# Optimization experiments

Hardware: AMD Instinct MI355X
Metric: run time of the kernel (lower is better)

## Reference

```python
import jax, jax.numpy as jnp
import numpy as np

N_EXPERTS = 64
TOP_K = 8
ALPHA = 0.01
EMBED_DIM = 2048


def setup_inputs() -> dict:
    key = jax.random.key(0)
    k1, k2 = jax.random.split(key)
    hidden_states = jax.random.normal(k1, (4, 8192, EMBED_DIM), dtype=jnp.float32)
    # router weight, torch init-style scale
    weight = jax.random.normal(k2, (N_EXPERTS, EMBED_DIM), dtype=jnp.float32) / np.sqrt(EMBED_DIM)
    return {"hidden_states": hidden_states, "weight": weight}


def reference(hidden_states, weight):
    # flatten tokens: [B,S,D] -> [N,D]
    x = hidden_states.reshape(-1, hidden_states.shape[-1])
    # router logits: [N,E]
    logits = jnp.einsum('nd,ed->ne', x, weight)
    scores = jax.nn.softmax(logits, axis=-1)
    # top-k routing weights and expert ids (torch uses sorted=False; order is immaterial)
    topk_weight, topk_idx = jax.lax.top_k(scores, TOP_K)
    # aux load-balance loss (training path, alpha > 0)
    counts = jnp.bincount(topk_idx.reshape(-1), length=N_EXPERTS).astype(scores.dtype)
    ce = counts / topk_idx.size  # fraction of assignments per expert
    Pi = scores.mean(axis=0)     # mean router prob per expert
    aux_loss = jnp.sum(Pi * ce * N_EXPERTS) * ALPHA
    return topk_idx, topk_weight, aux_loss
```

## Files before the change

### kernel.cpp

```cpp
#include <hip/hip_runtime.h>

#define EMBED_D  2048
#define N_EXP    64
#define K_TOP    8
#define TOK_BLK  64
#define THREADS  256
#define NCHUNK   64
#define WCHUNK_B 12288
#define XCHUNK_B 8192
#define BUF_B    (WCHUNK_B + XCHUNK_B)

typedef __attribute__((ext_vector_type(8))) short bf16x8;
typedef __attribute__((ext_vector_type(4))) float f32x4;

__device__ __forceinline__ uint bf16_rne(float x) {
    uint u = __float_as_uint(x);
    return (u + 0x7fffu + ((u >> 16) & 1u)) >> 16;
}
__device__ __forceinline__ float bf16f(uint h) { return __uint_as_float(h << 16); }

__device__ __forceinline__ void stage16(const void* g, void* l)
{
    typedef __attribute__((address_space(1))) const unsigned int gu32;
    typedef __attribute__((address_space(3))) unsigned int lu32;
    __builtin_amdgcn_global_load_lds((gu32*)g, (lu32*)l, 16, 0, 0);
}

__device__ __forceinline__ void split3(float4 u, float4 v, bf16x8& H, bf16x8& M, bf16x8& L)
{
    const float x[8] = {u.x, u.y, u.z, u.w, v.x, v.y, v.z, v.w};
    uint hw[8], mw[8], lw[8];
#pragma unroll
    for (int j = 0; j < 8; ++j) {
        const uint ux = __float_as_uint(x[j]);
        hw[j] = (ux + 0x7fffu + ((ux >> 16) & 1u)) & 0xffff0000u;
        const float r1 = x[j] - __uint_as_float(hw[j]);
        const uint ur = __float_as_uint(r1);
        mw[j] = (ur + 0x7fffu + ((ur >> 16) & 1u)) & 0xffff0000u;
        lw[j] = __float_as_uint(r1 - __uint_as_float(mw[j]));
    }
    uint* hp = (uint*)&H; uint* mp = (uint*)&M; uint* lp = (uint*)&L;
#pragma unroll
    for (int w = 0; w < 4; ++w) {
        hp[w] = __builtin_amdgcn_perm(hw[2 * w + 1], hw[2 * w], 0x07060302u);
        mp[w] = __builtin_amdgcn_perm(mw[2 * w + 1], mw[2 * w], 0x07060302u);
        lp[w] = __builtin_amdgcn_perm(lw[2 * w + 1], lw[2 * w], 0x07060302u);
    }
}

__global__ void w_prep(const float* __restrict__ W, ushort* __restrict__ WF)
{
    const int e = blockIdx.x;
    const int t = threadIdx.x;
    const float4 a = *(const float4*)(W + (size_t)e * EMBED_D + t * 8);
    const float4 b = *(const float4*)(W + (size_t)e * EMBED_D + t * 8 + 4);
    const float ev[8] = {a.x, a.y, a.z, a.w, b.x, b.y, b.z, b.w};
    ushort h[8], m[8], l[8];
#pragma unroll
    for (int j = 0; j < 8; ++j) {
        const uint hh = bf16_rne(ev[j]);
        const float r1 = ev[j] - bf16f(hh);
        const uint mm = bf16_rne(r1);
        const uint ll = bf16_rne(r1 - bf16f(mm));
        h[j] = (ushort)hh; m[j] = (ushort)mm; l[j] = (ushort)ll;
    }
    const int c = t >> 2;
    const int g = t & 3;
    const int lane = g * 16 + (e & 15);
    const int n    = e >> 4;
    const size_t base = (size_t)c * 6144 + (size_t)n * 512 + (size_t)lane * 8;
    ushort4* H = (ushort4*)(WF + base);
    ushort4* M = (ushort4*)(WF + base + 2048);
    ushort4* L = (ushort4*)(WF + base + 4096);
    H[0] = make_ushort4(h[0], h[1], h[2], h[3]); H[1] = make_ushort4(h[4], h[5], h[6], h[7]);
    M[0] = make_ushort4(m[0], m[1], m[2], m[3]); M[1] = make_ushort4(m[4], m[5], m[6], m[7]);
    L[0] = make_ushort4(l[0], l[1], l[2], l[3]); L[1] = make_ushort4(l[4], l[5], l[6], l[7]);
}

__global__ __launch_bounds__(THREADS, 4) void moe_gate_main(
    const float*  __restrict__ X,
    const ushort* __restrict__ WF,
    float* __restrict__ out,
    float* __restrict__ ws,
    int n_tok)
{
    __shared__ __align__(16) char smem[2 * BUF_B];
    __shared__ float sInvZ[TOK_BLK];
    __shared__ float sCnt[N_EXP];
    __shared__ float sColp[4][N_EXP];

    const int tid  = threadIdx.x;
    const int lane = tid & 63;
    const int wv   = __builtin_amdgcn_readfirstlane(tid >> 6);
    const int tg   = wv & 1;
    const int eh   = wv >> 1;
    const int row  = lane & 15;
    const int g    = lane >> 4;
    const int t0   = blockIdx.x * TOK_BLK;

    const char* wsrc = (const char*)WF + (size_t)wv * 1024 + lane * 16;
    const float* xsrc0; const float* xsrc1;
    {
        const int q0 = wv * 64 + lane,       t0k = q0 >> 3;
        const int q1 = 256 + wv * 64 + lane, t1k = q1 >> 3;
        xsrc0 = X + (size_t)(t0 + t0k) * EMBED_D + ((q0 & 7) ^ (t0k & 7)) * 4;
        xsrc1 = X + (size_t)(t0 + t1k) * EMBED_D + ((q1 & 7) ^ (t1k & 7)) * 4;
    }

    int xo[2][2];
#pragma unroll
    for (int ai = 0; ai < 2; ++ai) {
        const int tk = tg * 32 + ai * 16 + row;
        const int s  = tk & 7;
        xo[ai][0] = tk * 128 + ((2 * g)     ^ s) * 16;
        xo[ai][1] = tk * 128 + ((2 * g + 1) ^ s) * 16;
    }

    f32x4 acc[2][2];
#pragma unroll
    for (int ai = 0; ai < 2; ++ai)
#pragma unroll
        for (int nl = 0; nl < 2; ++nl)
            acc[ai][nl] = (f32x4){0.f, 0.f, 0.f, 0.f};

    {
        char* bb = smem;
#pragma unroll
        for (int r = 0; r < 3; ++r)
            stage16(wsrc + r * 4096, bb + r * 4096 + wv * 1024);
        stage16(xsrc0, bb + WCHUNK_B + wv * 1024);
        stage16(xsrc1, bb + WCHUNK_B + 4096 + wv * 1024);
    }
    __syncthreads();

    for (int c = 0; c < NCHUNK; ++c) {
        const int cur = c & 1;

        if (c + 1 < NCHUNK) {
            char* bb = smem + (cur ^ 1) * BUF_B;
            const char* wsc = wsrc + (size_t)(c + 1) * WCHUNK_B;
#pragma unroll
            for (int r = 0; r < 3; ++r)
                stage16(wsc + r * 4096, bb + r * 4096 + wv * 1024);
            stage16(xsrc0 + (c + 1) * 32, bb + WCHUNK_B + wv * 1024);
            stage16(xsrc1 + (c + 1) * 32, bb + WCHUNK_B + 4096 + wv * 1024);
        }

        const char* bb = smem + cur * BUF_B;
        const char* xb = bb + WCHUNK_B;

        bf16x8 ah[2], am[2], al[2];
#pragma unroll
        for (int ai = 0; ai < 2; ++ai) {
            const float4 u = *(const float4*)(xb + xo[ai][0]);
            const float4 v = *(const float4*)(xb + xo[ai][1]);
            split3(u, v, ah[ai], am[ai], al[ai]);
        }

#pragma unroll
        for (int nl = 0; nl < 2; ++nl) {
            const int n = eh * 2 + nl;
            const char* bp = bb + (size_t)n * 1024 + lane * 16;
            const bf16x8 bh = *(const bf16x8*)(bp);
            const bf16x8 bm = *(const bf16x8*)(bp + 4096);
            const bf16x8 bl = *(const bf16x8*)(bp + 8192);
#pragma unroll
            for (int ai = 0; ai < 2; ++ai) {
                acc[ai][nl] = __builtin_amdgcn_mfma_f32_16x16x32_bf16(ah[ai], bh, acc[ai][nl], 0, 0, 0);
                acc[ai][nl] = __builtin_amdgcn_mfma_f32_16x16x32_bf16(am[ai], bh, acc[ai][nl], 0, 0, 0);
                acc[ai][nl] = __builtin_amdgcn_mfma_f32_16x16x32_bf16(ah[ai], bm, acc[ai][nl], 0, 0, 0);
                acc[ai][nl] = __builtin_amdgcn_mfma_f32_16x16x32_bf16(al[ai], bh, acc[ai][nl], 0, 0, 0);
                acc[ai][nl] = __builtin_amdgcn_mfma_f32_16x16x32_bf16(ah[ai], bl, acc[ai][nl], 0, 0, 0);
                acc[ai][nl] = __builtin_amdgcn_mfma_f32_16x16x32_bf16(am[ai], bm, acc[ai][nl], 0, 0, 0);
            }
        }
        __syncthreads();
    }

    float (*Lp)[N_EXP + 1] = (float (*)[N_EXP + 1])smem;
#pragma unroll
    for (int ai = 0; ai < 2; ++ai)
#pragma unroll
        for (int nl = 0; nl < 2; ++nl)
#pragma unroll
            for (int r = 0; r < 4; ++r)
                Lp[tg * 32 + ai * 16 + g * 4 + r][(eh * 2 + nl) * 16 + row] = acc[ai][nl][r];
    if (tid < N_EXP) sCnt[tid] = 0.f;
    __syncthreads();

    if (tid < TOK_BLK) {
        const int t = tid;
        float mx = -1e30f;
        for (int e = 0; e < N_EXP; ++e)
            mx = fmaxf(mx, Lp[t][e]);
        float Z = 0.f;
        float tv[K_TOP]; int ti[K_TOP];
#pragma unroll
        for (int j = 0; j < K_TOP; ++j) { tv[j] = -1e30f; ti[j] = 0; }
        for (int e = 0; e < N_EXP; ++e) {
            const float s = __expf(Lp[t][e] - mx);
            Lp[t][e] = s;
            Z += s;
            float v = s; int id = e;
#pragma unroll
            for (int j = 0; j < K_TOP; ++j) {
                if (v > tv[j]) {
                    float fv = tv[j]; tv[j] = v; v = fv;
                    int   fi = ti[j]; ti[j] = id; id = fi;
                }
            }
        }
        const float invZ = 1.0f / Z;
        sInvZ[t] = invZ;
        const size_t ob = (size_t)(t0 + t) * K_TOP;
        const size_t wo = (size_t)n_tok * K_TOP;
#pragma unroll
        for (int j = 0; j < K_TOP; ++j) {
            out[ob + j]      = (float)ti[j];
            out[wo + ob + j] = tv[j] * invZ;
            atomicAdd(&sCnt[ti[j]], 1.0f);
        }
    }
    __syncthreads();

    {
        const int e = tid & 63, g2 = tid >> 6;
        float s = 0.f;
#pragma unroll
        for (int i = 0; i < 16; ++i) {
            const int t = g2 * 16 + i;
            s += Lp[t][e] * sInvZ[t];
        }
        sColp[g2][e] = s;
    }
    __syncthreads();
    if (tid < N_EXP) {
        float s = 0.f;
#pragma unroll
        for (int g2 = 0; g2 < 4; ++g2) s += sColp[g2][tid];
        atomicAdd(&ws[64 + tid], s);
        atomicAdd(&ws[tid], sCnt[tid]);
    }
}

__global__ void moe_aux(const float* __restrict__ ws, float* __restrict__ out, int n_tok)
{
    const int e = threadIdx.x;
    const float counts = ws[e];
    const float ssum   = ws[64 + e];
    const float Pi = ssum / (float)n_tok;
    const float ce = counts / ((float)n_tok * (float)K_TOP);
    float term = Pi * ce * (float)N_EXP;
    for (int off = 32; off; off >>= 1) term += __shfl_down(term, off);
    if (e == 0) out[(size_t)2 * n_tok * K_TOP] = term * 0.01f;
}

extern "C" void kernel_launch(void* const* d_in, const int* in_sizes, int n_in,
                              void* d_out, int out_size, void* d_ws, size_t ws_size,
                              hipStream_t stream)
{
    const float* X = (const float*)d_in[0];
    const float* W = (const float*)d_in[1];
    float* out = (float*)d_out;
    float* ws  = (float*)d_ws;
    const int n_tok = in_sizes[0] / EMBED_D;

    ushort* WF = (ushort*)(ws + 256);

    hipMemsetAsync(ws, 0, 2 * N_EXP * sizeof(float), stream);
    w_prep<<<N_EXP, 256, 0, stream>>>(W, WF);
    moe_gate_main<<<n_tok / TOK_BLK, THREADS, 0, stream>>>(X, WF, out, ws, n_tok);
    moe_aux<<<1, 64, 0, stream>>>(ws, out, n_tok);
}
```

Baseline: 419.3 us.

## Triple-buffer LDS pipeline with one barrier per chunk and per-wave token tiles

Moves the chunk loop from double to triple buffering with a prefetch distance of two. It waits on vmcnt before a single barrier per chunk instead of a trailing __syncthreads. Work is split so each wave owns 16 tokens across all 64 experts, so each wave splits only its own X slice once per chunk instead of two slices per wave. Occupancy hint drops from 4 to 2 blocks per CU and LDS use grows by half, trading fewer resident waves for deeper in-flight loads. The exact vmcnt(5) count assumes five outstanding loads per chunk, which ties correctness to the load count.

After: 421.7 us. About the same (+0.6%).

```diff
diff --git a/kernel.cpp b/kernel.cpp
--- a/kernel.cpp
+++ b/kernel.cpp
@@ -9,6 +9,7 @@
 #define WCHUNK_B 12288
 #define XCHUNK_B 8192
 #define BUF_B    (WCHUNK_B + XCHUNK_B)
+#define NBUF     3
 
 typedef __attribute__((ext_vector_type(8))) short bf16x8;
 typedef __attribute__((ext_vector_type(4))) float f32x4;
@@ -77,14 +78,14 @@
     L[0] = make_ushort4(l[0], l[1], l[2], l[3]); L[1] = make_ushort4(l[4], l[5], l[6], l[7]);
 }
 
-__global__ __launch_bounds__(THREADS, 4) void moe_gate_main(
+__global__ __launch_bounds__(THREADS, 2) void moe_gate_main(
     const float*  __restrict__ X,
     const ushort* __restrict__ WF,
     float* __restrict__ out,
     float* __restrict__ ws,
     int n_tok)
 {
-    __shared__ __align__(16) char smem[2 * BUF_B];
+    __shared__ __align__(16) char smem[NBUF * BUF_B];
     __shared__ float sInvZ[TOK_BLK];
     __shared__ float sCnt[N_EXP];
     __shared__ float sColp[4][N_EXP];
@@ -92,99 +93,88 @@
     const int tid  = threadIdx.x;
     const int lane = tid & 63;
     const int wv   = __builtin_amdgcn_readfirstlane(tid >> 6);
-    const int tg   = wv & 1;
-    const int eh   = wv >> 1;
     const int row  = lane & 15;
     const int g    = lane >> 4;
     const int t0   = blockIdx.x * TOK_BLK;
 
-    const char* wsrc = (const char*)WF + (size_t)wv * 1024 + lane * 16;
-    const float* xsrc0; const float* xsrc1;
+    const char* wsrc = (const char*)WF + (size_t)(wv * 1024) + lane * 16;
+    const float* xsrc[2];
     {
-        const int q0 = wv * 64 + lane,       t0k = q0 >> 3;
-        const int q1 = 256 + wv * 64 + lane, t1k = q1 >> 3;
-        xsrc0 = X + (size_t)(t0 + t0k) * EMBED_D + ((q0 & 7) ^ (t0k & 7)) * 4;
-        xsrc1 = X + (size_t)(t0 + t1k) * EMBED_D + ((q1 & 7) ^ (t1k & 7)) * 4;
-    }
-
-    int xo[2][2];
-#pragma unroll
-    for (int ai = 0; ai < 2; ++ai) {
-        const int tk = tg * 32 + ai * 16 + row;
-        const int s  = tk & 7;
-        xo[ai][0] = tk * 128 + ((2 * g)     ^ s) * 16;
-        xo[ai][1] = tk * 128 + ((2 * g + 1) ^ s) * 16;
-    }
-
-    f32x4 acc[2][2];
-#pragma unroll
-    for (int ai = 0; ai < 2; ++ai)
-#pragma unroll
-        for (int nl = 0; nl < 2; ++nl)
-            acc[ai][nl] = (f32x4){0.f, 0.f, 0.f, 0.f};
-
-    {
-        char* bb = smem;
+#pragma unroll
+        for (int i = 0; i < 2; ++i) {
+            const int s  = i * 64 + lane;
+            const int lt = s >> 1;
+            const int r  = (s & 1) ^ ((lt >> 2) & 1);
+            const int gg = lt >> 4, rr = lt & 15;
+            xsrc[i] = X + (size_t)(t0 + wv * 16 + rr) * EMBED_D + gg * 8 + r * 4;
+        }
+    }
+    const int c0  = (lane >> 2) & 1;
+    const int xo0 = (2 * lane + c0) * 16;
+    const int xo1 = (2 * lane + (c0 ^ 1)) * 16;
+
+    f32x4 acc[4];
+#pragma unroll
+    for (int n = 0; n < 4; ++n) acc[n] = (f32x4){0.f, 0.f, 0.f, 0.f};
+
+#pragma unroll
+    for (int c = 0; c < 2; ++c) {
+        char* bb = smem + c * BUF_B;
 #pragma unroll
         for (int r = 0; r < 3; ++r)
-            stage16(wsrc + r * 4096, bb + r * 4096 + wv * 1024);
-        stage16(xsrc0, bb + WCHUNK_B + wv * 1024);
-        stage16(xsrc1, bb + WCHUNK_B + 4096 + wv * 1024);
-    }
-    __syncthreads();
+            stage16(wsrc + (size_t)c * WCHUNK_B + r * 4096, bb + (r * 4 + wv) * 1024);
+#pragma unroll
+        for (int i = 0; i < 2; ++i)
+            stage16(xsrc[i] + c * 32, bb + WCHUNK_B + wv * 2048 + i * 1024);
+    }
 
     for (int c = 0; c < NCHUNK; ++c) {
-        const int cur = c & 1;
-
-        if (c + 1 < NCHUNK) {
-            char* bb = smem + (cur ^ 1) * BUF_B;
-            const char* wsc = wsrc + (size_t)(c + 1) * WCHUNK_B;
+        if (c + 1 < NCHUNK) asm volatile("s_waitcnt vmcnt(5)" ::: "memory");
+        else                asm volatile("s_waitcnt vmcnt(0)" ::: "memory");
+        __builtin_amdgcn_sched_barrier(0);
+        __builtin_amdgcn_s_barrier();
+
+        if (c + 2 < NCHUNK) {
+            char* bb = smem + ((c + 2) % NBUF) * BUF_B;
 #pragma unroll
             for (int r = 0; r < 3; ++r)
-                stage16(wsc + r * 4096, bb + r * 4096 + wv * 1024);
-            stage16(xsrc0 + (c + 1) * 32, bb + WCHUNK_B + wv * 1024);
-            stage16(xsrc1 + (c + 1) * 32, bb + WCHUNK_B + 4096 + wv * 1024);
-        }
-
-        const char* bb = smem + cur * BUF_B;
-        const char* xb = bb + WCHUNK_B;
-
-        bf16x8 ah[2], am[2], al[2];
-#pragma unroll
-        for (int ai = 0; ai < 2; ++ai) {
-            const float4 u = *(const float4*)(xb + xo[ai][0]);
-            const float4 v = *(const float4*)(xb + xo[ai][1]);
-            split3(u, v, ah[ai], am[ai], al[ai]);
-        }
-
-#pragma unroll
-        for (int nl = 0; nl < 2; ++nl) {
-            const int n = eh * 2 + nl;
-            const char* bp = bb + (size_t)n * 1024 + lane * 16;
+                stage16(wsrc + (size_t)(c + 2) * WCHUNK_B + r * 4096, bb + (r * 4 + wv) * 1024);
+#pragma unroll
+            for (int i = 0; i < 2; ++i)
+                stage16(xsrc[i] + (c + 2) * 32, bb + WCHUNK_B + wv * 2048 + i * 1024);
+        }
+
+        const char* bb = smem + (c % NBUF) * BUF_B;
+        const char* xb = bb + WCHUNK_B + wv * 2048;
+
+        bf16x8 ah, am, al;
+        {
+            const float4 u = *(const float4*)(xb + xo0);
+            const float4 v = *(const float4*)(xb + xo1);
+            split3(u, v, ah, am, al);
+        }
+#pragma unroll
+        for (int n = 0; n < 4; ++n) {
+            const char* bp = bb + n * 1024 + lane * 16;
             const bf16x8 bh = *(const bf16x8*)(bp);
             const bf16x8 bm = *(const bf16x8*)(bp + 4096);
             const bf16x8 bl = *(const bf16x8*)(bp + 8192);
-#pragma unroll
-            for (int ai = 0; ai < 2; ++ai) {
-                acc[ai][nl] = __builtin_amdgcn_mfma_f32_16x16x32_bf16(ah[ai], bh, acc[ai][nl], 0, 0, 0);
-                acc[ai][nl] = __builtin_amdgcn_mfma_f32_16x16x32_bf16(am[ai], bh, acc[ai][nl], 0, 0, 0);
-                acc[ai][nl] = __builtin_amdgcn_mfma_f32_16x16x32_bf16(ah[ai], bm, acc[ai][nl], 0, 0, 0);
-                acc[ai][nl] = __builtin_amdgcn_mfma_f32_16x16x32_bf16(al[ai], bh, acc[ai][nl], 0, 0, 0);
-                acc[ai][nl] = __builtin_amdgcn_mfma_f32_16x16x32_bf16(ah[ai], bl, acc[ai][nl], 0, 0, 0);
-                acc[ai][nl] = __builtin_amdgcn_mfma_f32_16x16x32_bf16(am[ai], bm, acc[ai][nl], 0, 0, 0);
-            }
-        }
-        __syncthreads();
-    }
+            acc[n] = __builtin_amdgcn_mfma_f32_16x16x32_bf16(ah, bh, acc[n], 0, 0, 0);
+            acc[n] = __builtin_amdgcn_mfma_f32_16x16x32_bf16(am, bh, acc[n], 0, 0, 0);
+            acc[n] = __builtin_amdgcn_mfma_f32_16x16x32_bf16(ah, bm, acc[n], 0, 0, 0);
+            acc[n] = __builtin_amdgcn_mfma_f32_16x16x32_bf16(al, bh, acc[n], 0, 0, 0);
+            acc[n] = __builtin_amdgcn_mfma_f32_16x16x32_bf16(ah, bl, acc[n], 0, 0, 0);
+            acc[n] = __builtin_amdgcn_mfma_f32_16x16x32_bf16(am, bm, acc[n], 0, 0, 0);
+        }
+    }
+    __syncthreads();
 
     float (*Lp)[N_EXP + 1] = (float (*)[N_EXP + 1])smem;
 #pragma unroll
-    for (int ai = 0; ai < 2; ++ai)
-#pragma unroll
-        for (int nl = 0; nl < 2; ++nl)
-#pragma unroll
-            for (int r = 0; r < 4; ++r)
-                Lp[tg * 32 + ai * 16 + g * 4 + r][(eh * 2 + nl) * 16 + row] = acc[ai][nl][r];
+    for (int n = 0; n < 4; ++n)
+#pragma unroll
+        for (int r = 0; r < 4; ++r)
+            Lp[wv * 16 + g * 4 + r][n * 16 + row] = acc[n][r];
     if (tid < N_EXP) sCnt[tid] = 0.f;
     __syncthreads();
 
```
